# Kernel tuning notes

Measured on AMD Instinct MI355X. Metric: run time of the kernel, lower is better.

Reference implementation:

```python
import jax, jax.numpy as jnp
import numpy as np

N = 524288      # total nodes
B = 4096        # number of graphs (segments)
D = 128         # input_dim
H = 256         # nb_hidden


def setup_inputs() -> dict:
    key = jax.random.key(0)
    ks = jax.random.split(key, 10)
    X = jax.random.normal(ks[0], (N, D), jnp.float32)
    # sorted, contiguous, non-empty segment ids (pyg `batch` vector)
    batch = ((jnp.arange(N) * B) // N).astype(jnp.int32)
    s = 0.05
    W0 = jax.random.normal(ks[1], (D, H), jnp.float32) * s
    b0 = jnp.zeros((H,), jnp.float32)
    W1 = jax.random.normal(ks[2], (H, H), jnp.float32) * s
    b1 = jnp.zeros((H,), jnp.float32)
    W2 = jax.random.normal(ks[3], (H, H), jnp.float32) * s
    b2 = jnp.zeros((H,), jnp.float32)
    Wf = jax.random.normal(ks[4], (H, 1), jnp.float32) * s
    bf = jnp.zeros((1,), jnp.float32)
    return {"X": X, "W0": W0, "b0": b0, "W1": W1, "b1": b1,
            "W2": W2, "b2": b2, "Wf": Wf, "bf": bf, "batch": batch}


def reference(X, W0, b0, W1, b1, W2, b2, Wf, bf, batch):
    # MLP logits (nb_layers=3 hidden Linear+ReLU, then final Linear to 1)
    h = jax.nn.relu(X @ W0 + b0)
    h = jax.nn.relu(h @ W1 + b1)
    h = jax.nn.relu(h @ W2 + b2)
    logits = (h @ Wf + bf)[:, 0]                          # [N]

    # batched_softmax: exp -> segment add -> gather -> div (as in original)
    e = jnp.exp(logits)
    seg_sum = jax.ops.segment_sum(e, batch, num_segments=B)   # [B]
    probs = e / seg_sum[batch]                                # [N]

    # batched_sample: per-segment categorical sample via Gumbel-max
    skey = jax.random.key(42)
    u = jax.random.uniform(skey, (N,), jnp.float32, 1e-20, 1.0)
    g = -jnp.log(-jnp.log(u))
    score = jnp.log(probs) + g                                # [N]
    seg_max = jax.ops.segment_max(score, batch, num_segments=B)
    winner = jnp.where(score >= seg_max[batch], jnp.arange(N), -1)
    shifted_actions = jax.ops.segment_max(winner, batch, num_segments=B)  # global idx per segment [B]
    p = probs[shifted_actions]                                # [B]

    # get_batch_shift: start offset of each segment
    counts = jax.ops.segment_sum(jnp.ones((N,), jnp.int32), batch, num_segments=B)
    starts = jnp.concatenate([jnp.zeros((1,), jnp.int32), jnp.cumsum(counts)[:-1]])
    actions = shifted_actions - starts                        # [B] local index within graph
    return (p, actions, shifted_actions)
```

## Files before the change

kernel.cpp:

```cpp
#include <hip/hip_runtime.h>
#include <hip/hip_bf16.h>


#define NFULL 524288
#define BSEG  4096
#define SEGSZ 128
#define DIN   128
#define HID   256
#define MROWS 128
#define KPAD  264

typedef __bf16 bf16x8 __attribute__((ext_vector_type(8)));
typedef float  f32x4  __attribute__((ext_vector_type(4)));

__device__ __forceinline__ unsigned short f2bf(float f) {
  __hip_bfloat16 h = __float2bfloat16(f);
  return __builtin_bit_cast(unsigned short, h);
}

__global__ __launch_bounds__(256) void convert_weights(
    const float* __restrict__ W0, const float* __restrict__ W1,
    const float* __restrict__ W2,
    unsigned short* __restrict__ W0t, unsigned short* __restrict__ W1t,
    unsigned short* __restrict__ W2t) {
  const int tid = blockIdx.x * 256 + threadIdx.x;
  if (tid < 32768) {
    const int n = tid >> 7, k = tid & 127;
    W0t[tid] = f2bf(W0[k * 256 + n]);
  } else if (tid < 98304) {
    const int u = tid - 32768;
    const int n = u >> 8, k = u & 255;
    W1t[u] = f2bf(W1[k * 256 + n]);
  } else if (tid < 163840) {
    const int u = tid - 98304;
    const int n = u >> 8, k = u & 255;
    W2t[u] = f2bf(W2[k * 256 + n]);
  }
}


template<int K>
__device__ __forceinline__ void do_layer(
    unsigned short* Abuf, const unsigned short* __restrict__ Wt,
    const float* __restrict__ bias, int w, int lane, f32x4 (&acc)[8][4]) {
  const int l15 = lane & 15;
  const int q   = lane >> 4;
  #pragma unroll
  for (int ni = 0; ni < 4; ++ni) {
    const float bv = bias[w * 64 + ni * 16 + l15];
    f32x4 c; c[0] = bv; c[1] = bv; c[2] = bv; c[3] = bv;
    #pragma unroll
    for (int mi = 0; mi < 8; ++mi) acc[mi][ni] = c;
  }
  const unsigned short* Ab = Abuf + l15 * KPAD + q * 8;
  const unsigned short* Bb = Wt + (w * 64 + l15) * K + q * 8;
  for (int k0 = 0; k0 < K; k0 += 32) {
    bf16x8 b[4];
    #pragma unroll
    for (int ni = 0; ni < 4; ++ni)
      b[ni] = *(const bf16x8*)(Bb + ni * 16 * K + k0);
    #pragma unroll
    for (int mi = 0; mi < 8; ++mi) {
      const bf16x8 a = *(const bf16x8*)(Ab + mi * 16 * KPAD + k0);
      #pragma unroll
      for (int ni = 0; ni < 4; ++ni)
        acc[mi][ni] = __builtin_amdgcn_mfma_f32_16x16x32_bf16(
            a, b[ni], acc[mi][ni], 0, 0, 0);
    }
  }
}

__device__ __forceinline__ void writeback_relu(
    unsigned short* Abuf, int w, int lane, const f32x4 (&acc)[8][4]) {
  const int l15 = lane & 15, q = lane >> 4;
  #pragma unroll
  for (int mi = 0; mi < 8; ++mi)
    #pragma unroll
    for (int ni = 0; ni < 4; ++ni) {
      const int col = w * 64 + ni * 16 + l15;
      #pragma unroll
      for (int r = 0; r < 4; ++r) {
        const int row = mi * 16 + q * 4 + r;
        Abuf[row * KPAD + col] = f2bf(fmaxf(acc[mi][ni][r], 0.f));
      }
    }
}

__global__ __launch_bounds__(256, 2) void mlp_mfma(
    const float* __restrict__ X,
    const unsigned short* __restrict__ W0t,
    const unsigned short* __restrict__ W1t,
    const unsigned short* __restrict__ W2t,
    const float* __restrict__ b0, const float* __restrict__ b1,
    const float* __restrict__ b2,
    const float* __restrict__ Wf, const float* __restrict__ bfp,
    float* __restrict__ logits) {
  __shared__ alignas(16) unsigned short Abuf[MROWS * KPAD];
  __shared__ float WfS[HID];
  __shared__ float Lpart[4][MROWS];
  const int tid  = threadIdx.x;
  const int lane = tid & 63;
  const int w    = tid >> 6;
  const size_t row0 = (size_t)blockIdx.x * MROWS;

  if (tid < HID) WfS[tid] = Wf[tid];

  {
    const int k4 = (tid & 31) * 4;
    int r = tid >> 5;
    #pragma unroll
    for (int it = 0; it < 16; ++it, r += 8) {
      const float4 v = *(const float4*)&X[(row0 + r) * DIN + k4];
      ushort4 p;
      p.x = f2bf(v.x); p.y = f2bf(v.y); p.z = f2bf(v.z); p.w = f2bf(v.w);
      *(ushort4*)&Abuf[r * KPAD + k4] = p;
    }
  }
  __syncthreads();

  f32x4 acc[8][4];
  do_layer<DIN>(Abuf, W0t, b0, w, lane, acc);
  __syncthreads();
  writeback_relu(Abuf, w, lane, acc);
  __syncthreads();
  do_layer<HID>(Abuf, W1t, b1, w, lane, acc);
  __syncthreads();
  writeback_relu(Abuf, w, lane, acc);
  __syncthreads();
  do_layer<HID>(Abuf, W2t, b2, w, lane, acc);

  const int l15 = lane & 15, q = lane >> 4;
  #pragma unroll
  for (int mi = 0; mi < 8; ++mi) {
    float part[4] = {0.f, 0.f, 0.f, 0.f};
    #pragma unroll
    for (int ni = 0; ni < 4; ++ni) {
      const float wf = WfS[w * 64 + ni * 16 + l15];
      #pragma unroll
      for (int r = 0; r < 4; ++r)
        part[r] = fmaf(fmaxf(acc[mi][ni][r], 0.f), wf, part[r]);
    }
    #pragma unroll
    for (int m = 1; m < 16; m <<= 1)
      #pragma unroll
      for (int r = 0; r < 4; ++r) part[r] += __shfl_xor(part[r], m, 16);
    if (l15 == 0)
      #pragma unroll
      for (int r = 0; r < 4; ++r) Lpart[w][mi * 16 + q * 4 + r] = part[r];
  }
  __syncthreads();
  if (tid < MROWS)
    logits[row0 + tid] = Lpart[0][tid] + Lpart[1][tid] + Lpart[2][tid] +
                         Lpart[3][tid] + bfp[0];
}

__device__ __forceinline__ void threefry2x32_42(unsigned x0, unsigned x1,
                                                unsigned& o0, unsigned& o1) {
  const unsigned ks0 = 0u, ks1 = 42u;
  const unsigned ks2 = ks0 ^ ks1 ^ 0x1BD11BDAu;
  x0 += ks0; x1 += ks1;
#define TF_R(r) { x0 += x1; x1 = (x1 << (r)) | (x1 >> (32 - (r))); x1 ^= x0; }
  TF_R(13) TF_R(15) TF_R(26) TF_R(6)   x0 += ks1; x1 += ks2 + 1u;
  TF_R(17) TF_R(29) TF_R(16) TF_R(24)  x0 += ks2; x1 += ks0 + 2u;
  TF_R(13) TF_R(15) TF_R(26) TF_R(6)   x0 += ks0; x1 += ks1 + 3u;
  TF_R(17) TF_R(29) TF_R(16) TF_R(24)  x0 += ks1; x1 += ks2 + 4u;
  TF_R(13) TF_R(15) TF_R(26) TF_R(6)   x0 += ks2; x1 += ks0 + 5u;
#undef TF_R
  o0 = x0; o1 = x1;
}

__global__ __launch_bounds__(128) void sample_kernel(
    const float* __restrict__ logits, float* __restrict__ out) {
  const int s = blockIdx.x;
  const int t = threadIdx.x;
  const int gi = s * SEGSZ + t;
  __shared__ float red[2];
  __shared__ float smax_sh[2];
  __shared__ int   sidx_sh[2];
  __shared__ float probs_sh[SEGSZ];
  const int wave = t >> 6;

  const float lg = logits[gi];
  const float e  = expf(lg);

  float v = e;
  #pragma unroll
  for (int off = 32; off >= 1; off >>= 1) v += __shfl_xor(v, off, 64);
  if ((t & 63) == 0) red[wave] = v;
  __syncthreads();
  const float S = red[0] + red[1];
  const float prob = e / S;
  probs_sh[t] = prob;

  unsigned o0, o1;
  threefry2x32_42(0u, (unsigned)gi, o0, o1);
  const float f = __uint_as_float(0x3f800000u | (o0 >> 9)) - 1.0f;
  const float u = fmaxf(1e-20f, f + 1e-20f);
  const float g = -logf(-logf(u));
  float score = logf(prob) + g;

  float ms = score; int mi = gi;
  #pragma unroll
  for (int off = 1; off < 64; off <<= 1) {
    const float os = __shfl_xor(ms, off, 64);
    const int   oi = __shfl_xor(mi, off, 64);
    if (os > ms || (os == ms && oi > mi)) { ms = os; mi = oi; }
  }
  if ((t & 63) == 0) { smax_sh[wave] = ms; sidx_sh[wave] = mi; }
  __syncthreads();
  if (t == 0) {
    const float s0 = smax_sh[0], s1 = smax_sh[1];
    const int   i0 = sidx_sh[0], i1 = sidx_sh[1];
    const int win = (s1 > s0 || (s1 == s0 && i1 > i0)) ? i1 : i0;
    out[s]            = probs_sh[win - s * SEGSZ];
    out[BSEG + s]     = (float)(win - s * SEGSZ);
    out[2 * BSEG + s] = (float)win;
  }
}

extern "C" void kernel_launch(void* const* d_in, const int* in_sizes, int n_in,
                              void* d_out, int out_size, void* d_ws, size_t ws_size,
                              hipStream_t stream) {
  const float* X  = (const float*)d_in[0];
  const float* W0 = (const float*)d_in[1];
  const float* b0 = (const float*)d_in[2];
  const float* W1 = (const float*)d_in[3];
  const float* b1 = (const float*)d_in[4];
  const float* W2 = (const float*)d_in[5];
  const float* b2 = (const float*)d_in[6];
  const float* Wf = (const float*)d_in[7];
  const float* bf = (const float*)d_in[8];

  float* logits = (float*)d_ws;
  unsigned short* W0t = (unsigned short*)((char*)d_ws + (size_t)NFULL * 4);
  unsigned short* W1t = W0t + 256 * 128;
  unsigned short* W2t = W1t + 256 * 256;
  float* out = (float*)d_out;

  convert_weights<<<640, 256, 0, stream>>>(W0, W1, W2, W0t, W1t, W2t);
  mlp_mfma<<<NFULL / MROWS, 256, 0, stream>>>(X, W0t, W1t, W2t, b0, b1, b2,
                                              Wf, bf, logits);
  sample_kernel<<<BSEG, 128, 0, stream>>>(logits, out);
}
```

Baseline: 531.8 us.

## Fuse segment softmax sampling into MLP kernel with 8-wave 2D tiling

Merges the MLP and the per-segment softmax/Gumbel sampling into one kernel, since each 128-row block is exactly one segment. This removes the logits round trip through global memory and one launch. It also moves from 4 to 8 waves per block, each owning a 64x64 output tile instead of 128x64, which halves accumulator registers. The MFMA operands are swapped so the weights come first and the accumulator is transposed, which allows vectorized ushort4 writeback and float4 bias loads. The risk is more LDS read traffic per MFMA and tail work done by only 128 of 512 threads.

Measured after the change: 656.4 us. 23.4% more time.

```diff
diff --git a/kernel.cpp b/kernel.cpp
--- a/kernel.cpp
+++ b/kernel.cpp
@@ -41,117 +41,55 @@
 
 template<int K>
 __device__ __forceinline__ void do_layer(
-    unsigned short* Abuf, const unsigned short* __restrict__ Wt,
-    const float* __restrict__ bias, int w, int lane, f32x4 (&acc)[8][4]) {
+    const unsigned short* Abuf, const unsigned short* __restrict__ Wt,
+    const float* __restrict__ bias, int wq, int wr, int lane,
+    f32x4 (&acc)[4][4]) {
   const int l15 = lane & 15;
   const int q   = lane >> 4;
   #pragma unroll
-  for (int ni = 0; ni < 4; ++ni) {
-    const float bv = bias[w * 64 + ni * 16 + l15];
-    f32x4 c; c[0] = bv; c[1] = bv; c[2] = bv; c[3] = bv;
-    #pragma unroll
-    for (int mi = 0; mi < 8; ++mi) acc[mi][ni] = c;
-  }
-  const unsigned short* Ab = Abuf + l15 * KPAD + q * 8;
-  const unsigned short* Bb = Wt + (w * 64 + l15) * K + q * 8;
+  for (int ct = 0; ct < 4; ++ct) {
+    const float4 bv4 = *(const float4*)&bias[wq * 64 + ct * 16 + q * 4];
+    f32x4 c; c[0] = bv4.x; c[1] = bv4.y; c[2] = bv4.z; c[3] = bv4.w;
+    #pragma unroll
+    for (int rt = 0; rt < 4; ++rt) acc[ct][rt] = c;
+  }
+  const unsigned short* Wb = Wt + (wq * 64 + l15) * K + q * 8;
+  const unsigned short* Ab = Abuf + (wr * 64 + l15) * KPAD + q * 8;
+  #pragma unroll 2
   for (int k0 = 0; k0 < K; k0 += 32) {
-    bf16x8 b[4];
-    #pragma unroll
-    for (int ni = 0; ni < 4; ++ni)
-      b[ni] = *(const bf16x8*)(Bb + ni * 16 * K + k0);
-    #pragma unroll
-    for (int mi = 0; mi < 8; ++mi) {
-      const bf16x8 a = *(const bf16x8*)(Ab + mi * 16 * KPAD + k0);
+    bf16x8 wv[4], rv[4];
+    #pragma unroll
+    for (int ct = 0; ct < 4; ++ct)
+      wv[ct] = *(const bf16x8*)(Wb + ct * 16 * K + k0);
+    #pragma unroll
+    for (int rt = 0; rt < 4; ++rt)
+      rv[rt] = *(const bf16x8*)(Ab + rt * 16 * KPAD + k0);
+    #pragma unroll
+    for (int ct = 0; ct < 4; ++ct)
       #pragma unroll
-      for (int ni = 0; ni < 4; ++ni)
-        acc[mi][ni] = __builtin_amdgcn_mfma_f32_16x16x32_bf16(
-            a, b[ni], acc[mi][ni], 0, 0, 0);
-    }
+      for (int rt = 0; rt < 4; ++rt)
+        acc[ct][rt] = __builtin_amdgcn_mfma_f32_16x16x32_bf16(
+            wv[ct], rv[rt], acc[ct][rt], 0, 0, 0);
   }
 }
 
 __device__ __forceinline__ void writeback_relu(
-    unsigned short* Abuf, int w, int lane, const f32x4 (&acc)[8][4]) {
+    unsigned short* Abuf, int wq, int wr, int lane, const f32x4 (&acc)[4][4]) {
   const int l15 = lane & 15, q = lane >> 4;
   #pragma unroll
-  for (int mi = 0; mi < 8; ++mi)
-    #pragma unroll
-    for (int ni = 0; ni < 4; ++ni) {
-      const int col = w * 64 + ni * 16 + l15;
-      #pragma unroll
-      for (int r = 0; r < 4; ++r) {
-        const int row = mi * 16 + q * 4 + r;
-        Abuf[row * KPAD + col] = f2bf(fmaxf(acc[mi][ni][r], 0.f));
-      }
-    }
-}
-
-__global__ __launch_bounds__(256, 2) void mlp_mfma(
-    const float* __restrict__ X,
-    const unsigned short* __restrict__ W0t,
-    const unsigned short* __restrict__ W1t,
-    const unsigned short* __restrict__ W2t,
-    const float* __restrict__ b0, const float* __restrict__ b1,
-    const float* __restrict__ b2,
-    const float* __restrict__ Wf, const float* __restrict__ bfp,
-    float* __restrict__ logits) {
-  __shared__ alignas(16) unsigned short Abuf[MROWS * KPAD];
-  __shared__ float WfS[HID];
-  __shared__ float Lpart[4][MROWS];
-  const int tid  = threadIdx.x;
-  const int lane = tid & 63;
-  const int w    = tid >> 6;
-  const size_t row0 = (size_t)blockIdx.x * MROWS;
-
-  if (tid < HID) WfS[tid] = Wf[tid];
-
-  {
-    const int k4 = (tid & 31) * 4;
-    int r = tid >> 5;
-    #pragma unroll
-    for (int it = 0; it < 16; ++it, r += 8) {
-      const float4 v = *(const float4*)&X[(row0 + r) * DIN + k4];
+  for (int rt = 0; rt < 4; ++rt) {
+    const int row = wr * 64 + rt * 16 + l15;
+    #pragma unroll
+    for (int ct = 0; ct < 4; ++ct) {
+      const int col = wq * 64 + ct * 16 + q * 4;
       ushort4 p;
-      p.x = f2bf(v.x); p.y = f2bf(v.y); p.z = f2bf(v.z); p.w = f2bf(v.w);
-      *(ushort4*)&Abuf[r * KPAD + k4] = p;
-    }
-  }
-  __syncthreads();
-
-  f32x4 acc[8][4];
-  do_layer<DIN>(Abuf, W0t, b0, w, lane, acc);
-  __syncthreads();
-  writeback_relu(Abuf, w, lane, acc);
-  __syncthreads();
-  do_layer<HID>(Abuf, W1t, b1, w, lane, acc);
-  __syncthreads();
-  writeback_relu(Abuf, w, lane, acc);
-  __syncthreads();
-  do_layer<HID>(Abuf, W2t, b2, w, lane, acc);
-
-  const int l15 = lane & 15, q = lane >> 4;
-  #pragma unroll
-  for (int mi = 0; mi < 8; ++mi) {
-    float part[4] = {0.f, 0.f, 0.f, 0.f};
-    #pragma unroll
-    for (int ni = 0; ni < 4; ++ni) {
-      const float wf = WfS[w * 64 + ni * 16 + l15];
-      #pragma unroll
-      for (int r = 0; r < 4; ++r)
-        part[r] = fmaf(fmaxf(acc[mi][ni][r], 0.f), wf, part[r]);
-    }
-    #pragma unroll
-    for (int m = 1; m < 16; m <<= 1)
-      #pragma unroll
-      for (int r = 0; r < 4; ++r) part[r] += __shfl_xor(part[r], m, 16);
-    if (l15 == 0)
-      #pragma unroll
-      for (int r = 0; r < 4; ++r) Lpart[w][mi * 16 + q * 4 + r] = part[r];
-  }
-  __syncthreads();
-  if (tid < MROWS)
-    logits[row0 + tid] = Lpart[0][tid] + Lpart[1][tid] + Lpart[2][tid] +
-                         Lpart[3][tid] + bfp[0];
+      p.x = f2bf(fmaxf(acc[ct][rt][0], 0.f));
+      p.y = f2bf(fmaxf(acc[ct][rt][1], 0.f));
+      p.z = f2bf(fmaxf(acc[ct][rt][2], 0.f));
+      p.w = f2bf(fmaxf(acc[ct][rt][3], 0.f));
+      *(ushort4*)&Abuf[row * KPAD + col] = p;
+    }
+  }
 }
 
 __device__ __forceinline__ void threefry2x32_42(unsigned x0, unsigned x1,
@@ -169,52 +107,125 @@
   o0 = x0; o1 = x1;
 }
 
-__global__ __launch_bounds__(128) void sample_kernel(
-    const float* __restrict__ logits, float* __restrict__ out) {
-  const int s = blockIdx.x;
-  const int t = threadIdx.x;
-  const int gi = s * SEGSZ + t;
+__global__ __launch_bounds__(512, 4) void mlp_fused(
+    const float* __restrict__ X,
+    const unsigned short* __restrict__ W0t,
+    const unsigned short* __restrict__ W1t,
+    const unsigned short* __restrict__ W2t,
+    const float* __restrict__ b0, const float* __restrict__ b1,
+    const float* __restrict__ b2,
+    const float* __restrict__ Wf, const float* __restrict__ bfp,
+    float* __restrict__ out) {
+  __shared__ alignas(16) unsigned short Abuf[MROWS * KPAD];
+  __shared__ float WfS[HID];
+  __shared__ float Lpart[8][64];
+  __shared__ float logit_sh[MROWS];
   __shared__ float red[2];
   __shared__ float smax_sh[2];
   __shared__ int   sidx_sh[2];
-  __shared__ float probs_sh[SEGSZ];
-  const int wave = t >> 6;
-
-  const float lg = logits[gi];
-  const float e  = expf(lg);
-
-  float v = e;
+  const int tid  = threadIdx.x;
+  const int lane = tid & 63;
+  const int w    = tid >> 6;
+  const int wq   = w & 3;
+  const int wr   = w >> 2;
+  const int l15  = lane & 15;
+  const int q    = lane >> 4;
+  const int seg  = blockIdx.x;
+  const size_t row0 = (size_t)seg * MROWS;
+
+  if (tid < HID) WfS[tid] = Wf[tid];
+
   #pragma unroll
-  for (int off = 32; off >= 1; off >>= 1) v += __shfl_xor(v, off, 64);
-  if ((t & 63) == 0) red[wave] = v;
-  __syncthreads();
-  const float S = red[0] + red[1];
-  const float prob = e / S;
-  probs_sh[t] = prob;
-
-  unsigned o0, o1;
-  threefry2x32_42(0u, (unsigned)gi, o0, o1);
-  const float f = __uint_as_float(0x3f800000u | (o0 >> 9)) - 1.0f;
-  const float u = fmaxf(1e-20f, f + 1e-20f);
-  const float g = -logf(-logf(u));
-  float score = logf(prob) + g;
-
-  float ms = score; int mi = gi;
-  #pragma unroll
-  for (int off = 1; off < 64; off <<= 1) {
-    const float os = __shfl_xor(ms, off, 64);
-    const int   oi = __shfl_xor(mi, off, 64);
-    if (os > ms || (os == ms && oi > mi)) { ms = os; mi = oi; }
-  }
-  if ((t & 63) == 0) { smax_sh[wave] = ms; sidx_sh[wave] = mi; }
-  __syncthreads();
-  if (t == 0) {
+  for (int it = 0; it < 8; ++it) {
+    const int idx = tid + it * 512;
+    const int r   = idx >> 5;
+    const int k4  = (idx & 31) * 4;
+    const float4 v = *(const float4*)&X[(row0 + r) * DIN + k4];
+    ushort4 p;
+    p.x = f2bf(v.x); p.y = f2bf(v.y); p.z = f2bf(v.z); p.w = f2bf(v.w);
+    *(ushort4*)&Abuf[r * KPAD + k4] = p;
+  }
+  __syncthreads();
+
+  f32x4 acc[4][4];
+  do_layer<DIN>(Abuf, W0t, b0, wq, wr, lane, acc);
+  __syncthreads();
+  writeback_relu(Abuf, wq, wr, lane, acc);
+  __syncthreads();
+  do_layer<HID>(Abuf, W1t, b1, wq, wr, lane, acc);
+  __syncthreads();
+  writeback_relu(Abuf, wq, wr, lane, acc);
+  __syncthreads();
+  do_layer<HID>(Abuf, W2t, b2, wq, wr, lane, acc);
+
+  {
+    float part[4];
+    #pragma unroll
+    for (int rt = 0; rt < 4; ++rt) {
+      float p = 0.f;
+      #pragma unroll
+      for (int ct = 0; ct < 4; ++ct) {
+        const int col = wq * 64 + ct * 16 + q * 4;
+        #pragma unroll
+        for (int r = 0; r < 4; ++r)
+          p = fmaf(fmaxf(acc[ct][rt][r], 0.f), WfS[col + r], p);
+      }
+      part[rt] = p;
+    }
+    #pragma unroll
+    for (int rt = 0; rt < 4; ++rt) {
+      part[rt] += __shfl_xor(part[rt], 16, 64);
+      part[rt] += __shfl_xor(part[rt], 32, 64);
+    }
+    if (q == 0)
+      #pragma unroll
+      for (int rt = 0; rt < 4; ++rt) Lpart[w][rt * 16 + l15] = part[rt];
+  }
+  __syncthreads();
+  if (tid < MROWS) {
+    const int g = (tid >> 6) * 4;
+    const int r = tid & 63;
+    logit_sh[tid] = Lpart[g][r] + Lpart[g + 1][r] + Lpart[g + 2][r] +
+                    Lpart[g + 3][r] + bfp[0];
+  }
+  __syncthreads();
+
+  float e = 0.f, score = 0.f, prob = 0.f;
+  if (tid < SEGSZ) {
+    e = expf(logit_sh[tid]);
+    float v = e;
+    #pragma unroll
+    for (int off = 32; off >= 1; off >>= 1) v += __shfl_xor(v, off, 64);
+    if ((tid & 63) == 0) red[tid >> 6] = v;
+  }
+  __syncthreads();
+  if (tid < SEGSZ) {
+    const float S = red[0] + red[1];
+    prob = e / S;
+    unsigned o0, o1;
+    threefry2x32_42(0u, (unsigned)(row0 + tid), o0, o1);
+    const float f = __uint_as_float(0x3f800000u | (o0 >> 9)) - 1.0f;
+    const float u = fmaxf(1e-20f, f + 1e-20f);
+    const float g = -logf(-logf(u));
+    score = logf(prob) + g;
+    logit_sh[tid] = prob;
+    float ms = score; int mi = tid;
+    #pragma unroll
+    for (int off = 1; off < 64; off <<= 1) {
+      const float os = __shfl_xor(ms, off, 64);
+      const int   oi = __shfl_xor(mi, off, 64);
+      if (os > ms || (os == ms && oi > mi)) { ms = os; mi = oi; }
+    }
+    if ((tid & 63) == 0) { smax_sh[tid >> 6] = ms; sidx_sh[tid >> 6] = mi; }
+  }
+  __syncthreads();
+  if (tid == 0) {
     const float s0 = smax_sh[0], s1 = smax_sh[1];
     const int   i0 = sidx_sh[0], i1 = sidx_sh[1];
     const int win = (s1 > s0 || (s1 == s0 && i1 > i0)) ? i1 : i0;
-    out[s]            = probs_sh[win - s * SEGSZ];
-    out[BSEG + s]     = (float)(win - s * SEGSZ);
-    out[2 * BSEG + s] = (float)win;
+    out[seg]            = logit_sh[win];
+    out[BSEG + seg]     = (float)win;
+    out[2 * BSEG + seg] = (float)(row0 + win);
   }
 }
 
@@ -231,14 +242,12 @@
   const float* Wf = (const float*)d_in[7];
   const float* bf = (const float*)d_in[8];
 
-  float* logits = (float*)d_ws;
-  unsigned short* W0t = (unsigned short*)((char*)d_ws + (size_t)NFULL * 4);
+  unsigned short* W0t = (unsigned short*)d_ws;
   unsigned short* W1t = W0t + 256 * 128;
   unsigned short* W2t = W1t + 256 * 256;
   float* out = (float*)d_out;
 
   convert_weights<<<640, 256, 0, stream>>>(W0, W1, W2, W0t, W1t, W2t);
-  mlp_mfma<<<NFULL / MROWS, 256, 0, stream>>>(X, W0t, W1t, W2t, b0, b1, b2,
-                                              Wf, bf, logits);
-  sample_kernel<<<BSEG, 128, 0, stream>>>(logits, out);
-}
+  mlp_fused<<<BSEG, 512, 0, stream>>>(X, W0t, W1t, W2t, b0, b1, b2,
+                                      Wf, bf, out);
+}
```
